# Kernel tuning notes

Measured on AMD Instinct MI355X. Metric: run time of the kernel, lower is better.

Reference implementation:

```python
import jax, jax.numpy as jnp
import numpy as np
from functools import partial

N_QUBITS = 4
N_LAYERS = 2
DIM = 2 ** N_QUBITS  # 16


def _conv(x, w, b):
    y = jax.lax.conv_general_dilated(
        x, w, window_strides=(1, 1), padding='SAME',
        dimension_numbers=('NCHW', 'OIHW', 'NCHW'))
    return y + b[None, :, None, None]


def _maxpool2(x):
    return jax.lax.reduce_window(
        x, -jnp.inf, jax.lax.max,
        window_dimensions=(1, 1, 2, 2), window_strides=(1, 1, 2, 2), padding='VALID')


def _rot_matrix(phi, theta, omega):
    # Rot = RZ(omega) @ RY(theta) @ RZ(phi)
    c = jnp.cos(theta / 2).astype(jnp.complex64)
    s = jnp.sin(theta / 2).astype(jnp.complex64)
    ep = jnp.exp(-0.5j * (phi + omega).astype(jnp.complex64))
    em = jnp.exp(0.5j * (phi - omega).astype(jnp.complex64))
    row0 = jnp.stack([ep * c, -em * s])
    row1 = jnp.stack([jnp.conj(em) * s, jnp.conj(ep) * c])
    return jnp.stack([row0, row1])  # [2,2]


def _quantum_circuit(feat16, q_weights):
    # feat16: [B,16] real; amplitude embedding with normalization
    B = feat16.shape[0]
    norm = jnp.linalg.norm(feat16, axis=1, keepdims=True)
    amps = feat16 / jnp.maximum(norm, 1e-12)
    state = amps.astype(jnp.complex64).reshape((B,) + (2,) * N_QUBITS)
    for layer in range(N_LAYERS):
        for q in range(N_QUBITS):
            U = _rot_matrix(q_weights[layer, q, 0], q_weights[layer, q, 1], q_weights[layer, q, 2])
            state = jnp.moveaxis(jnp.tensordot(U, state, axes=[[1], [q + 1]]), 0, q + 1)
        for q in range(N_QUBITS - 1):
            # CNOT control=q, target=q+1 (adjacent wires)
            s = state.reshape(B, 2 ** q, 2, 2, 2 ** (N_QUBITS - q - 2))
            s = s.at[:, :, 1].set(s[:, :, 1, ::-1])
            state = s.reshape((B,) + (2,) * N_QUBITS)
    probs = jnp.real(state * jnp.conj(state))  # [B,2,2,2,2]
    outs = []
    for q in range(N_QUBITS):
        axes = tuple(a for a in range(1, N_QUBITS + 1) if a != q + 1)
        p = probs.sum(axis=axes)  # [B,2]
        outs.append(p[:, 0] - p[:, 1])  # <Z_q>
    return jnp.stack(outs, axis=1)  # [B,4]


def _forward(x, conv1_w, conv1_b, conv2_w, conv2_b, fc1_w, fc1_b, fc2_w, fc2_b,
             fc3_w, fc3_b, q_weights, fc4_w, fc4_b):
    h = jax.nn.relu(_conv(x, conv1_w, conv1_b))
    h = _maxpool2(h)  # [B,32,14,14]
    h = jax.nn.relu(_conv(h, conv2_w, conv2_b))
    h = _maxpool2(h)  # [B,64,7,7]
    h = h.reshape(h.shape[0], 64 * 7 * 7)
    h = jax.nn.relu(h @ fc1_w.T + fc1_b)
    h = jax.nn.relu(h @ fc2_w.T + fc2_b)
    feat = jax.nn.relu(h @ fc3_w.T + fc3_b)  # [B,16]
    q_out = _quantum_circuit(feat, q_weights)  # [B,4]
    z = jnp.concatenate([feat, q_out], axis=1) @ fc4_w.T + fc4_b  # [B,10]
    return jax.nn.log_softmax(z, axis=1)


def setup_inputs() -> dict:
    key = jax.random.key(0)
    ks = jax.random.split(key, 16)
    B = 1024
    def g(k, shape, fan_in):
        return jax.random.normal(k, shape, dtype=jnp.float32) * (1.0 / np.sqrt(fan_in))
    return {
        'x': jax.random.normal(ks[0], (B, 1, 28, 28), dtype=jnp.float32),
        'conv1_w': g(ks[1], (32, 1, 3, 3), 9),
        'conv1_b': jnp.zeros((32,), jnp.float32),
        'conv2_w': g(ks[2], (64, 32, 3, 3), 32 * 9),
        'conv2_b': jnp.zeros((64,), jnp.float32),
        'fc1_w': g(ks[3], (128, 64 * 7 * 7), 64 * 7 * 7),
        'fc1_b': jnp.zeros((128,), jnp.float32),
        'fc2_w': g(ks[4], (64, 128), 128),
        'fc2_b': jnp.zeros((64,), jnp.float32),
        'fc3_w': g(ks[5], (16, 64), 64),
        'fc3_b': jnp.zeros((16,), jnp.float32),
        'q_weights': jax.random.normal(ks[6], (N_LAYERS, N_QUBITS, 3), dtype=jnp.float32),
        'fc4_w': g(ks[7], (10, 16 + N_QUBITS), 20),
        'fc4_b': jnp.zeros((10,), jnp.float32),
    }


def reference(x, conv1_w, conv1_b, conv2_w, conv2_b, fc1_w, fc1_b, fc2_w, fc2_b,
              fc3_w, fc3_b, q_weights, fc4_w, fc4_b):
    return _forward(x, conv1_w, conv1_b, conv2_w, conv2_b, fc1_w, fc1_b,
                    fc2_w, fc2_b, fc3_w, fc3_b, q_weights, fc4_w, fc4_b)
```

## Files before the change

kernel.cpp:

```cpp
#include <hip/hip_runtime.h>
#include <math.h>

typedef unsigned short ushort_t;
typedef unsigned int uint_t;
typedef __attribute__((ext_vector_type(8))) short short8v;
typedef __attribute__((ext_vector_type(4))) float float4v;
typedef __attribute__((ext_vector_type(4))) unsigned short ushort4v;

static __device__ __forceinline__ ushort_t f2bf(float f) {
    union { float f; uint_t u; } v; v.f = f;
    uint_t r = (v.u + 0x7FFFu + ((v.u >> 16) & 1u)) >> 16;
    return (ushort_t)r;
}
static __device__ __forceinline__ float bf2f(ushort_t u) {
    union { uint_t u; float f; } v; v.u = ((uint_t)u) << 16;
    return v.f;
}

__global__ __launch_bounds__(256) void k_conv(
    const float* __restrict__ x,
    const float* __restrict__ c1w, const float* __restrict__ c1b,
    const float* __restrict__ c2w, const float* __restrict__ c2b,
    const float* __restrict__ fc1w, ushort_t* __restrict__ wb,
    ushort_t* __restrict__ p2g)
{
    const int t = threadIdx.x;
    if (blockIdx.x >= 1024) {
        const int i = ((blockIdx.x - 1024)*256 + t) * 8;
        const float4 a = *(const float4*)(fc1w + i);
        const float4 b = *(const float4*)(fc1w + i + 4);
        short8v pk;
        pk[0]=(short)f2bf(a.x); pk[1]=(short)f2bf(a.y);
        pk[2]=(short)f2bf(a.z); pk[3]=(short)f2bf(a.w);
        pk[4]=(short)f2bf(b.x); pk[5]=(short)f2bf(b.y);
        pk[6]=(short)f2bf(b.z); pk[7]=(short)f2bf(b.w);
        *(short8v*)(wb + i) = pk;
        return;
    }

    __shared__ __align__(16) ushort_t p1cl[8192];
    __shared__ __align__(16) float img[900];

    const int b = blockIdx.x;
    const int lane = t & 63, wv = t >> 6;

    for (int i = t; i < 4096; i += 256) ((uint_t*)p1cl)[i] = 0u;
    for (int i = t; i < 900; i += 256) img[i] = 0.f;
    __syncthreads();
    const float* xi = x + (size_t)b * 784;
    for (int i = t; i < 784; i += 256)
        img[(i/28 + 1)*30 + (i%28 + 1)] = xi[i];
    __syncthreads();

    {
        const int ocb1 = wv*8;
        float wk[8][9], bv[8];
        #pragma unroll
        for (int o = 0; o < 8; ++o) {
            bv[o] = c1b[ocb1 + o];
            #pragma unroll
            for (int k = 0; k < 9; ++k) wk[o][k] = c1w[(ocb1 + o)*9 + k];
        }
        #pragma unroll
        for (int ch = 0; ch < 4; ++ch) {
            int pos = ch*64 + lane;
            const bool act = pos < 196;
            if (!act) pos = 195;
            const int qy = pos / 14, qx = pos % 14;
            const float* ib = img + (2*qy)*30 + 2*qx;
            float v[4][4];
            #pragma unroll
            for (int rr = 0; rr < 4; ++rr) {
                const float2 a = *(const float2*)(ib + rr*30);
                const float2 c = *(const float2*)(ib + rr*30 + 2);
                v[rr][0]=a.x; v[rr][1]=a.y; v[rr][2]=c.x; v[rr][3]=c.y;
            }
            short8v pk;
            #pragma unroll
            for (int o = 0; o < 8; ++o) {
                float m = 0.f;
                #pragma unroll
                for (int dy = 0; dy < 2; ++dy)
                #pragma unroll
                for (int dx = 0; dx < 2; ++dx) {
                    float acc = bv[o];
                    #pragma unroll
                    for (int ky = 0; ky < 3; ++ky)
                    #pragma unroll
                    for (int kx = 0; kx < 3; ++kx)
                        acc = fmaf(v[dy+ky][dx+kx], wk[o][ky*3+kx], acc);
                    m = fmaxf(m, acc);
                }
                pk[o] = (short)f2bf(m);
            }
            if (act) *(short8v*)&p1cl[wv*2048 + ((qy+1)*16 + (qx+1))*8] = pk;
        }
    }
    __syncthreads();

    {
        const int ocb = wv*16;
        const int col = lane & 15, g = lane >> 4;
        const int oc  = ocb + col;
        short8v bfr[9];
        #pragma unroll
        for (int j = 0; j < 8; ++j) {
            const float* wp = c2w + ((size_t)oc*32 + g*8 + j)*9;
            #pragma unroll
            for (int s = 0; s < 9; ++s) bfr[s][j] = (short)f2bf(wp[s]);
        }
        const float bv = c2b[oc];
        ushort_t* po = p2g + (size_t)b*3136;
        #pragma unroll 1
        for (int mt = 0; mt < 13; ++mt) {
            int row = mt*16 + col; if (row > 195) row = 195;
            const int q  = row >> 2;
            const int py = q / 7, px = q - py*7;
            const int y0 = 2*py + ((row>>1)&1), x0 = 2*px + (row&1);
            const ushort_t* ap = &p1cl[g*2048 + (y0*16 + x0)*8];
            float4v c0 = {bv, bv, bv, bv};
            float4v c1 = {0.f, 0.f, 0.f, 0.f};
            c0 = __builtin_amdgcn_mfma_f32_16x16x32_bf16(*(const short8v*)(ap +   0), bfr[0], c0, 0, 0, 0);
            c1 = __builtin_amdgcn_mfma_f32_16x16x32_bf16(*(const short8v*)(ap +   8), bfr[1], c1, 0, 0, 0);
            c0 = __builtin_amdgcn_mfma_f32_16x16x32_bf16(*(const short8v*)(ap +  16), bfr[2], c0, 0, 0, 0);
            c1 = __builtin_amdgcn_mfma_f32_16x16x32_bf16(*(const short8v*)(ap + 128), bfr[3], c1, 0, 0, 0);
            c0 = __builtin_amdgcn_mfma_f32_16x16x32_bf16(*(const short8v*)(ap + 136), bfr[4], c0, 0, 0, 0);
            c1 = __builtin_amdgcn_mfma_f32_16x16x32_bf16(*(const short8v*)(ap + 144), bfr[5], c1, 0, 0, 0);
            c0 = __builtin_amdgcn_mfma_f32_16x16x32_bf16(*(const short8v*)(ap + 256), bfr[6], c0, 0, 0, 0);
            c1 = __builtin_amdgcn_mfma_f32_16x16x32_bf16(*(const short8v*)(ap + 264), bfr[7], c1, 0, 0, 0);
            c0 = __builtin_amdgcn_mfma_f32_16x16x32_bf16(*(const short8v*)(ap + 272), bfr[8], c0, 0, 0, 0);
            const int quad = mt*4 + g;
            if (quad < 49) {
                const float m0 = fmaxf(fmaxf(c0[0]+c1[0], c0[1]+c1[1]),
                                       fmaxf(c0[2]+c1[2], c0[3]+c1[3]));
                po[oc*49 + quad] = f2bf(fmaxf(m0, 0.f));
            }
        }
    }
}

__global__ __launch_bounds__(256) void k_fc1(
    const ushort_t* __restrict__ p2g, const ushort_t* __restrict__ wb,
    const float* __restrict__ fc1b, float* __restrict__ h1g)
{
    __shared__ float cred[4][16][16];
    const int t = threadIdx.x, lane = t & 63, wv = t >> 6;
    const int imgT = blockIdx.x, ocT = blockIdx.y;
    const int sel = lane & 15, koff = (lane >> 4) * 8;
    const ushort_t* arow = p2g + (size_t)(imgT*16 + sel)*3136;
    const ushort_t* brow = wb  + (size_t)(ocT*16 + sel)*3136;
    const int n    = (wv < 2) ? 25 : 24;
    const int kbeg = wv*24 + (wv < 2 ? wv : 2);
    float4v c = {0.f, 0.f, 0.f, 0.f};
    int k0 = kbeg*32 + koff;
    short8v a0 = *(const short8v*)(arow + k0);
    short8v b0 = *(const short8v*)(brow + k0);
    for (int kk = 1; kk < n; ++kk) {
        const int k1 = (kbeg + kk)*32 + koff;
        const short8v a1 = *(const short8v*)(arow + k1);
        const short8v b1 = *(const short8v*)(brow + k1);
        c = __builtin_amdgcn_mfma_f32_16x16x32_bf16(a0, b0, c, 0, 0, 0);
        a0 = a1; b0 = b1;
    }
    c = __builtin_amdgcn_mfma_f32_16x16x32_bf16(a0, b0, c, 0, 0, 0);
    #pragma unroll
    for (int r = 0; r < 4; ++r) cred[wv][(lane>>4)*4 + r][sel] = c[r];
    __syncthreads();
    const int m = t >> 4, nn = t & 15;
    const float s = cred[0][m][nn] + cred[1][m][nn] + cred[2][m][nn] + cred[3][m][nn]
                  + fc1b[ocT*16 + nn];
    h1g[(size_t)(imgT*16 + m)*128 + ocT*16 + nn] = fmaxf(s, 0.f);
}

__global__ __launch_bounds__(64) void k_head(
    const float* __restrict__ h1,
    const float* __restrict__ fc2w, const float* __restrict__ fc2b,
    const float* __restrict__ fc3w, const float* __restrict__ fc3b,
    const float* __restrict__ qw,
    const float* __restrict__ fc4w, const float* __restrict__ fc4b,
    float* __restrict__ out)
{
    __shared__ float h1s[4][132];
    __shared__ float h2s[4][68];
    __shared__ float fs[4][16];
    __shared__ float zs[4][12];
    const int t = threadIdx.x;
    const int r = t >> 4, l = t & 15;
    const int b0 = blockIdx.x * 4;
    for (int i = t; i < 4*128; i += 64) h1s[i>>7][i&127] = h1[(size_t)b0*128 + i];
    __syncthreads();

    const int o0 = l*4;
    float a0 = fc2b[o0+0], a1 = fc2b[o0+1], a2 = fc2b[o0+2], a3 = fc2b[o0+3];
    #pragma unroll 4
    for (int k4 = 0; k4 < 32; ++k4) {
        const float4 h  = *(const float4*)&h1s[r][k4*4];
        const float4 w0 = *(const float4*)&fc2w[(o0+0)*128 + k4*4];
        const float4 w1 = *(const float4*)&fc2w[(o0+1)*128 + k4*4];
        const float4 w2 = *(const float4*)&fc2w[(o0+2)*128 + k4*4];
        const float4 w3 = *(const float4*)&fc2w[(o0+3)*128 + k4*4];
        a0 = fmaf(h.x,w0.x,fmaf(h.y,w0.y,fmaf(h.z,w0.z,fmaf(h.w,w0.w,a0))));
        a1 = fmaf(h.x,w1.x,fmaf(h.y,w1.y,fmaf(h.z,w1.z,fmaf(h.w,w1.w,a1))));
        a2 = fmaf(h.x,w2.x,fmaf(h.y,w2.y,fmaf(h.z,w2.z,fmaf(h.w,w2.w,a2))));
        a3 = fmaf(h.x,w3.x,fmaf(h.y,w3.y,fmaf(h.z,w3.z,fmaf(h.w,w3.w,a3))));
    }
    {
        float4 v = make_float4(fmaxf(a0,0.f), fmaxf(a1,0.f), fmaxf(a2,0.f), fmaxf(a3,0.f));
        *(float4*)&h2s[r][o0] = v;
    }
    __syncthreads();

    float facc = fc3b[l];
    #pragma unroll 4
    for (int k4 = 0; k4 < 16; ++k4) {
        const float4 h  = *(const float4*)&h2s[r][k4*4];
        const float4 wv = *(const float4*)&fc3w[l*64 + k4*4];
        facc = fmaf(h.x,wv.x,fmaf(h.y,wv.y,fmaf(h.z,wv.z,fmaf(h.w,wv.w,facc))));
    }
    const float feat = fmaxf(facc, 0.f);
    fs[r][l] = feat;

    float nrm2 = feat*feat;
    nrm2 += __shfl_xor(nrm2, 1);
    nrm2 += __shfl_xor(nrm2, 2);
    nrm2 += __shfl_xor(nrm2, 4);
    nrm2 += __shfl_xor(nrm2, 8);
    const float nrm = fmaxf(sqrtf(nrm2), 1e-12f);
    float re = feat / nrm, im = 0.f;
    #pragma unroll
    for (int layer = 0; layer < 2; ++layer) {
        #pragma unroll
        for (int q = 0; q < 4; ++q) {
            const float phi = qw[(layer*4 + q)*3 + 0];
            const float th  = qw[(layer*4 + q)*3 + 1];
            const float om  = qw[(layer*4 + q)*3 + 2];
            float st, ct; sincosf(0.5f*th, &st, &ct);
            float sa, ca; sincosf(0.5f*(phi + om), &sa, &ca);
            float sb, cb; sincosf(0.5f*(phi - om), &sb, &cb);
            const int pbit = 3 - q;
            const int bit  = (l >> pbit) & 1;
            const float pre = __shfl_xor(re, 1 << pbit);
            const float pim = __shfl_xor(im, 1 << pbit);
            const float sel = bit ? 1.f : -1.f;
            const float coR = ca*ct;
            const float coI = sel*sa*ct;
            const float cpR = sel*cb*st;
            const float cpI = -sb*st;
            const float nr = coR*re - coI*im + cpR*pre - cpI*pim;
            const float ni = coR*im + coI*re + cpR*pim + cpI*pre;
            re = nr; im = ni;
        }
        #pragma unroll
        for (int q = 0; q < 3; ++q) {
            const int cbit = 3 - q, tbit = 2 - q;
            const float sre = __shfl_xor(re, 1 << tbit);
            const float sim = __shfl_xor(im, 1 << tbit);
            if ((l >> cbit) & 1) { re = sre; im = sim; }
        }
    }
    const float pr = fmaf(re, re, im*im);
    float qo[4];
    #pragma unroll
    for (int q = 0; q < 4; ++q) {
        float v = ((l >> (3-q)) & 1) ? -pr : pr;
        v += __shfl_xor(v, 1);
        v += __shfl_xor(v, 2);
        v += __shfl_xor(v, 4);
        v += __shfl_xor(v, 8);
        qo[q] = v;
    }
    __syncthreads();

    if (l < 10) {
        float z = fc4b[l];
        #pragma unroll
        for (int j = 0; j < 16; ++j) z = fmaf(fs[r][j], fc4w[l*20 + j], z);
        #pragma unroll
        for (int j = 0; j < 4; ++j)  z = fmaf(qo[j], fc4w[l*20 + 16 + j], z);
        zs[r][l] = z;
        float mx = zs[r][0];
        #pragma unroll
        for (int j = 1; j < 10; ++j) mx = fmaxf(mx, zs[r][j]);
        float se = 0.f;
        #pragma unroll
        for (int j = 0; j < 10; ++j) se += expf(zs[r][j] - mx);
        out[(size_t)(b0 + r)*10 + l] = z - mx - logf(se);
    }
}

static __device__ __forceinline__ void circuit_head(
    const float* feat_in, const float* __restrict__ qw,
    const float* __restrict__ fc4w, const float* __restrict__ fc4b,
    float* __restrict__ outp)
{
    float feat[16];
    #pragma unroll
    for (int j = 0; j < 16; ++j) feat[j] = feat_in[j];
    float nrm2 = 0.f;
    #pragma unroll
    for (int j = 0; j < 16; ++j) nrm2 += feat[j]*feat[j];
    const float inv = 1.f / fmaxf(sqrtf(nrm2), 1e-12f);
    float ar[16], ai[16];
    #pragma unroll
    for (int j = 0; j < 16; ++j) { ar[j] = feat[j]*inv; ai[j] = 0.f; }
    #pragma unroll
    for (int layer = 0; layer < 2; ++layer) {
        #pragma unroll
        for (int q = 0; q < 4; ++q) {
            const float phi = qw[(layer*4 + q)*3 + 0];
            const float th  = qw[(layer*4 + q)*3 + 1];
            const float om  = qw[(layer*4 + q)*3 + 2];
            float st, ct; sincosf(0.5f*th, &st, &ct);
            float sa, ca; sincosf(0.5f*(phi + om), &sa, &ca);
            float sb, cb; sincosf(0.5f*(phi - om), &sb, &cb);
            const float U00r =  ca*ct, U00i = -sa*ct;
            const float U01r = -cb*st, U01i = -sb*st;
            const float U10r =  cb*st, U10i = -sb*st;
            const float U11r =  ca*ct, U11i =  sa*ct;
            const int stride = 1 << (3 - q);
            #pragma unroll
            for (int i0 = 0; i0 < 16; ++i0) {
                if (i0 & stride) continue;
                const int i1 = i0 | stride;
                const float r0 = ar[i0], m0 = ai[i0];
                const float r1 = ar[i1], m1 = ai[i1];
                ar[i0] = U00r*r0 - U00i*m0 + U01r*r1 - U01i*m1;
                ai[i0] = U00r*m0 + U00i*r0 + U01r*m1 + U01i*r1;
                ar[i1] = U10r*r0 - U10i*m0 + U11r*r1 - U11i*m1;
                ai[i1] = U10r*m0 + U10i*r0 + U11r*m1 + U11i*r1;
            }
        }
        #pragma unroll
        for (int q = 0; q < 3; ++q) {
            const int cbit = 1 << (3 - q), tbit = 1 << (2 - q);
            #pragma unroll
            for (int idx = 0; idx < 16; ++idx) {
                if ((idx & cbit) && !(idx & tbit)) {
                    const int j = idx | tbit;
                    float tr = ar[idx]; ar[idx] = ar[j]; ar[j] = tr;
                    float ti = ai[idx]; ai[idx] = ai[j]; ai[j] = ti;
                }
            }
        }
    }
    float qo[4];
    #pragma unroll
    for (int q = 0; q < 4; ++q) {
        const int pb = 1 << (3 - q);
        float s = 0.f;
        #pragma unroll
        for (int idx = 0; idx < 16; ++idx) {
            const float pv = ar[idx]*ar[idx] + ai[idx]*ai[idx];
            s += (idx & pb) ? -pv : pv;
        }
        qo[q] = s;
    }
    float z[10];
    float mx = -1e30f;
    #pragma unroll
    for (int o = 0; o < 10; ++o) {
        float a = fc4b[o];
        #pragma unroll
        for (int j = 0; j < 16; ++j) a = fmaf(feat[j], fc4w[o*20 + j], a);
        #pragma unroll
        for (int j = 0; j < 4;  ++j) a = fmaf(qo[j],  fc4w[o*20 + 16 + j], a);
        z[o] = a; mx = fmaxf(mx, a);
    }
    float se = 0.f;
    #pragma unroll
    for (int o = 0; o < 10; ++o) se += expf(z[o] - mx);
    const float lse = logf(se);
    #pragma unroll
    for (int o = 0; o < 10; ++o) outp[o] = z[o] - mx - lse;
}

__global__ __launch_bounds__(256) void k_fused_b(
    const float* __restrict__ x,
    const float* __restrict__ c1w, const float* __restrict__ c1b,
    const float* __restrict__ c2w, const float* __restrict__ c2b,
    const ushort_t* __restrict__ fc1wb, const float* __restrict__ fc1b,
    const float* __restrict__ fc2w, const float* __restrict__ fc2b,
    const float* __restrict__ fc3w, const float* __restrict__ fc3b,
    const float* __restrict__ qw,
    const float* __restrict__ fc4w, const float* __restrict__ fc4b,
    float* __restrict__ out)
{
    __shared__ __align__(16) ushort_t p1cl[8192];
    __shared__ __align__(16) float p2[3136];
    __shared__ float h1s[128];
    __shared__ float h2s[64];
    __shared__ float fts[16];

    const int b = blockIdx.x, t = threadIdx.x;
    const int lane = t & 63, wv = t >> 6;

    for (int i = t; i < 4096; i += 256) ((uint_t*)p1cl)[i] = 0u;
    float* img = p2;
    for (int i = t; i < 900; i += 256) img[i] = 0.f;
    __syncthreads();
    const float* xi = x + (size_t)b * 784;
    for (int i = t; i < 784; i += 256)
        img[(i/28 + 1)*30 + (i%28 + 1)] = xi[i];
    __syncthreads();

    {
        const int ocb1 = wv*8;
        float wk[8][9], bv[8];
        #pragma unroll
        for (int o = 0; o < 8; ++o) {
            bv[o] = c1b[ocb1 + o];
            #pragma unroll
            for (int k = 0; k < 9; ++k) wk[o][k] = c1w[(ocb1 + o)*9 + k];
        }
        #pragma unroll
        for (int ch = 0; ch < 4; ++ch) {
            int pos = ch*64 + lane;
            const bool act = pos < 196;
            if (!act) pos = 195;
            const int qy = pos / 14, qx = pos % 14;
            const float* ib = img + (2*qy)*30 + 2*qx;
            float v[4][4];
            #pragma unroll
            for (int rr = 0; rr < 4; ++rr) {
                const float2 a = *(const float2*)(ib + rr*30);
                const float2 c = *(const float2*)(ib + rr*30 + 2);
                v[rr][0]=a.x; v[rr][1]=a.y; v[rr][2]=c.x; v[rr][3]=c.y;
            }
            short8v pk;
            #pragma unroll
            for (int o = 0; o < 8; ++o) {
                float m = 0.f;
                #pragma unroll
                for (int dy = 0; dy < 2; ++dy)
                #pragma unroll
                for (int dx = 0; dx < 2; ++dx) {
                    float acc = bv[o];
                    #pragma unroll
                    for (int ky = 0; ky < 3; ++ky)
                    #pragma unroll
                    for (int kx = 0; kx < 3; ++kx)
                        acc = fmaf(v[dy+ky][dx+kx], wk[o][ky*3+kx], acc);
                    m = fmaxf(m, acc);
                }
                pk[o] = (short)f2bf(m);
            }
            if (act) *(short8v*)&p1cl[wv*2048 + ((qy+1)*16 + (qx+1))*8] = pk;
        }
    }
    __syncthreads();

    {
        const int ocb = wv*16;
        const int col = lane & 15, g = lane >> 4;
        const int oc  = ocb + col;
        short8v bfr[9];
        #pragma unroll
        for (int j = 0; j < 8; ++j) {
            const float* wp = c2w + ((size_t)oc*32 + g*8 + j)*9;
            #pragma unroll
            for (int s = 0; s < 9; ++s) bfr[s][j] = (short)f2bf(wp[s]);
        }
        const float bv = c2b[oc];
        #pragma unroll 1
        for (int mt = 0; mt < 13; ++mt) {
            int row = mt*16 + col; if (row > 195) row = 195;
            const int q  = row >> 2;
            const int py = q / 7, px = q - py*7;
            const int y0 = 2*py + ((row>>1)&1), x0 = 2*px + (row&1);
            const ushort_t* ap = &p1cl[g*2048 + (y0*16 + x0)*8];
            float4v c0 = {bv, bv, bv, bv};
            float4v c1 = {0.f, 0.f, 0.f, 0.f};
            c0 = __builtin_amdgcn_mfma_f32_16x16x32_bf16(*(const short8v*)(ap +   0), bfr[0], c0, 0, 0, 0);
            c1 = __builtin_amdgcn_mfma_f32_16x16x32_bf16(*(const short8v*)(ap +   8), bfr[1], c1, 0, 0, 0);
            c0 = __builtin_amdgcn_mfma_f32_16x16x32_bf16(*(const short8v*)(ap +  16), bfr[2], c0, 0, 0, 0);
            c1 = __builtin_amdgcn_mfma_f32_16x16x32_bf16(*(const short8v*)(ap + 128), bfr[3], c1, 0, 0, 0);
            c0 = __builtin_amdgcn_mfma_f32_16x16x32_bf16(*(const short8v*)(ap + 136), bfr[4], c0, 0, 0, 0);
            c1 = __builtin_amdgcn_mfma_f32_16x16x32_bf16(*(const short8v*)(ap + 144), bfr[5], c1, 0, 0, 0);
            c0 = __builtin_amdgcn_mfma_f32_16x16x32_bf16(*(const short8v*)(ap + 256), bfr[6], c0, 0, 0, 0);
            c1 = __builtin_amdgcn_mfma_f32_16x16x32_bf16(*(const short8v*)(ap + 264), bfr[7], c1, 0, 0, 0);
            c0 = __builtin_amdgcn_mfma_f32_16x16x32_bf16(*(const short8v*)(ap + 272), bfr[8], c0, 0, 0, 0);
            const int quad = mt*4 + g;
            if (quad < 49) {
                const float m0 = fmaxf(fmaxf(c0[0]+c1[0], c0[1]+c1[1]),
                                       fmaxf(c0[2]+c1[2], c0[3]+c1[3]));
                p2[oc*49 + quad] = fmaxf(m0, 0.f);
            }
        }
    }
    __syncthreads();

    for (int pass = 0; pass < 8; ++pass) {
        const int o = wv*32 + pass*4;
        const ushort_t* w0 = fc1wb + (size_t)o*3136;
        float a0=0.f, a1=0.f, a2=0.f, a3=0.f;
        #pragma unroll 2
        for (int kb = 0; kb < 3072; kb += 256) {
            const int k = kb + lane*4;
            const float4 pv = *(const float4*)&p2[k];
            const ushort4v u0 = *(const ushort4v*)(w0 + k);
            const ushort4v u1 = *(const ushort4v*)(w0 + 3136 + k);
            const ushort4v u2 = *(const ushort4v*)(w0 + 6272 + k);
            const ushort4v u3 = *(const ushort4v*)(w0 + 9408 + k);
            a0 = fmaf(pv.x,bf2f(u0[0]),fmaf(pv.y,bf2f(u0[1]),fmaf(pv.z,bf2f(u0[2]),fmaf(pv.w,bf2f(u0[3]),a0))));
            a1 = fmaf(pv.x,bf2f(u1[0]),fmaf(pv.y,bf2f(u1[1]),fmaf(pv.z,bf2f(u1[2]),fmaf(pv.w,bf2f(u1[3]),a1))));
            a2 = fmaf(pv.x,bf2f(u2[0]),fmaf(pv.y,bf2f(u2[1]),fmaf(pv.z,bf2f(u2[2]),fmaf(pv.w,bf2f(u2[3]),a2))));
            a3 = fmaf(pv.x,bf2f(u3[0]),fmaf(pv.y,bf2f(u3[1]),fmaf(pv.z,bf2f(u3[2]),fmaf(pv.w,bf2f(u3[3]),a3))));
        }
        if (lane < 16) {
            const int k = 3072 + lane*4;
            const float4 pv = *(const float4*)&p2[k];
            const ushort4v u0 = *(const ushort4v*)(w0 + k);
            const ushort4v u1 = *(const ushort4v*)(w0 + 3136 + k);
            const ushort4v u2 = *(const ushort4v*)(w0 + 6272 + k);
            const ushort4v u3 = *(const ushort4v*)(w0 + 9408 + k);
            a0 = fmaf(pv.x,bf2f(u0[0]),fmaf(pv.y,bf2f(u0[1]),fmaf(pv.z,bf2f(u0[2]),fmaf(pv.w,bf2f(u0[3]),a0))));
            a1 = fmaf(pv.x,bf2f(u1[0]),fmaf(pv.y,bf2f(u1[1]),fmaf(pv.z,bf2f(u1[2]),fmaf(pv.w,bf2f(u1[3]),a1))));
            a2 = fmaf(pv.x,bf2f(u2[0]),fmaf(pv.y,bf2f(u2[1]),fmaf(pv.z,bf2f(u2[2]),fmaf(pv.w,bf2f(u2[3]),a2))));
            a3 = fmaf(pv.x,bf2f(u3[0]),fmaf(pv.y,bf2f(u3[1]),fmaf(pv.z,bf2f(u3[2]),fmaf(pv.w,bf2f(u3[3]),a3))));
        }
        #pragma unroll
        for (int s = 1; s < 64; s <<= 1) {
            a0 += __shfl_xor(a0, s);
            a1 += __shfl_xor(a1, s);
            a2 += __shfl_xor(a2, s);
            a3 += __shfl_xor(a3, s);
        }
        if (lane == ((o+0)&63)) h1s[o+0] = fmaxf(a0 + fc1b[o+0], 0.f);
        if (lane == ((o+1)&63)) h1s[o+1] = fmaxf(a1 + fc1b[o+1], 0.f);
        if (lane == ((o+2)&63)) h1s[o+2] = fmaxf(a2 + fc1b[o+2], 0.f);
        if (lane == ((o+3)&63)) h1s[o+3] = fmaxf(a3 + fc1b[o+3], 0.f);
    }
    __syncthreads();

    if (t < 64) {
        float a = fc2b[t];
        const float* wr = fc2w + t * 128;
        for (int k = 0; k < 128; ++k) a = fmaf(h1s[k], wr[k], a);
        h2s[t] = fmaxf(a, 0.f);
    }
    __syncthreads();
    if (t < 16) {
        float a = fc3b[t];
        const float* wr = fc3w + t * 64;
        for (int k = 0; k < 64; ++k) a = fmaf(h2s[k], wr[k], a);
        fts[t] = fmaxf(a, 0.f);
    }
    __syncthreads();
    if (t == 0) circuit_head(fts, qw, fc4w, fc4b, out + (size_t)b*10);
}

__global__ __launch_bounds__(256) void k_cvtw_fb(
    const float* __restrict__ w, ushort_t* __restrict__ o)
{
    const int i = (blockIdx.x*256 + threadIdx.x) * 8;
    const float4 a = *(const float4*)(w + i);
    const float4 b = *(const float4*)(w + i + 4);
    short8v pk;
    pk[0]=(short)f2bf(a.x); pk[1]=(short)f2bf(a.y);
    pk[2]=(short)f2bf(a.z); pk[3]=(short)f2bf(a.w);
    pk[4]=(short)f2bf(b.x); pk[5]=(short)f2bf(b.y);
    pk[6]=(short)f2bf(b.z); pk[7]=(short)f2bf(b.w);
    *(short8v*)(o + i) = pk;
}

extern "C" void kernel_launch(void* const* d_in, const int* in_sizes, int n_in,
                              void* d_out, int out_size, void* d_ws, size_t ws_size,
                              hipStream_t stream) {
    const float* x     = (const float*)d_in[0];
    const float* c1w   = (const float*)d_in[1];
    const float* c1b   = (const float*)d_in[2];
    const float* c2w   = (const float*)d_in[3];
    const float* c2b   = (const float*)d_in[4];
    const float* fc1w  = (const float*)d_in[5];
    const float* fc1b  = (const float*)d_in[6];
    const float* fc2w  = (const float*)d_in[7];
    const float* fc2b  = (const float*)d_in[8];
    const float* fc3w  = (const float*)d_in[9];
    const float* fc3b  = (const float*)d_in[10];
    const float* qwp   = (const float*)d_in[11];
    const float* fc4w  = (const float*)d_in[12];
    const float* fc4b  = (const float*)d_in[13];
    float* outp = (float*)d_out;

    const size_t WB  = (size_t)128*3136*2;
    const size_t P2B = (size_t)1024*3136*2;
    const size_t H1B = (size_t)1024*128*4;

    if (ws_size >= WB + P2B + H1B) {
        ushort_t* wb  = (ushort_t*)d_ws;
        ushort_t* p2g = (ushort_t*)((char*)d_ws + WB);
        float*    h1g = (float*)((char*)d_ws + WB + P2B);
        k_conv<<<1220, 256, 0, stream>>>(x, c1w, c1b, c2w, c2b, fc1w, wb, p2g);
        k_fc1<<<dim3(64, 8), 256, 0, stream>>>(p2g, wb, fc1b, h1g);
        k_head<<<256, 64, 0, stream>>>(h1g, fc2w, fc2b, fc3w, fc3b, qwp,
                                       fc4w, fc4b, outp);
    } else if (ws_size >= WB) {
        ushort_t* wb = (ushort_t*)d_ws;
        k_cvtw_fb<<<196, 256, 0, stream>>>(fc1w, wb);
        k_fused_b<<<1024, 256, 0, stream>>>(x, c1w, c1b, c2w, c2b, wb, fc1b,
                                            fc2w, fc2b, fc3w, fc3b, qwp,
                                            fc4w, fc4b, outp);
    }
}
```

Baseline: 56.89 us.

## Fuse fc1 GEMM into head kernel, removing the h1 global round trip

Merges the fc1 MFMA GEMM and the fc2/fc3/quantum/fc4 head into one kernel with 64 blocks, each handling 16 images across all 128 fc1 outputs. The aim is to drop one kernel launch and the global write and read of the h1 activations. In exchange, the fc1 work runs on far fewer blocks. Each wave walks the full 98-step K loop with no K-split and no explicit prefetch, which lengthens the serial load-latency chain.

New measurement: 89.57 us. 57.4% more time.

```diff
diff --git a/kernel.cpp b/kernel.cpp
--- a/kernel.cpp
+++ b/kernel.cpp
@@ -139,56 +139,50 @@
     }
 }
 
-__global__ __launch_bounds__(256) void k_fc1(
+__global__ __launch_bounds__(256) void k_tail(
     const ushort_t* __restrict__ p2g, const ushort_t* __restrict__ wb,
-    const float* __restrict__ fc1b, float* __restrict__ h1g)
-{
-    __shared__ float cred[4][16][16];
-    const int t = threadIdx.x, lane = t & 63, wv = t >> 6;
-    const int imgT = blockIdx.x, ocT = blockIdx.y;
-    const int sel = lane & 15, koff = (lane >> 4) * 8;
-    const ushort_t* arow = p2g + (size_t)(imgT*16 + sel)*3136;
-    const ushort_t* brow = wb  + (size_t)(ocT*16 + sel)*3136;
-    const int n    = (wv < 2) ? 25 : 24;
-    const int kbeg = wv*24 + (wv < 2 ? wv : 2);
-    float4v c = {0.f, 0.f, 0.f, 0.f};
-    int k0 = kbeg*32 + koff;
-    short8v a0 = *(const short8v*)(arow + k0);
-    short8v b0 = *(const short8v*)(brow + k0);
-    for (int kk = 1; kk < n; ++kk) {
-        const int k1 = (kbeg + kk)*32 + koff;
-        const short8v a1 = *(const short8v*)(arow + k1);
-        const short8v b1 = *(const short8v*)(brow + k1);
-        c = __builtin_amdgcn_mfma_f32_16x16x32_bf16(a0, b0, c, 0, 0, 0);
-        a0 = a1; b0 = b1;
-    }
-    c = __builtin_amdgcn_mfma_f32_16x16x32_bf16(a0, b0, c, 0, 0, 0);
-    #pragma unroll
-    for (int r = 0; r < 4; ++r) cred[wv][(lane>>4)*4 + r][sel] = c[r];
-    __syncthreads();
-    const int m = t >> 4, nn = t & 15;
-    const float s = cred[0][m][nn] + cred[1][m][nn] + cred[2][m][nn] + cred[3][m][nn]
-                  + fc1b[ocT*16 + nn];
-    h1g[(size_t)(imgT*16 + m)*128 + ocT*16 + nn] = fmaxf(s, 0.f);
-}
-
-__global__ __launch_bounds__(64) void k_head(
-    const float* __restrict__ h1,
+    const float* __restrict__ fc1b,
     const float* __restrict__ fc2w, const float* __restrict__ fc2b,
     const float* __restrict__ fc3w, const float* __restrict__ fc3b,
     const float* __restrict__ qw,
     const float* __restrict__ fc4w, const float* __restrict__ fc4b,
     float* __restrict__ out)
 {
-    __shared__ float h1s[4][132];
-    __shared__ float h2s[4][68];
-    __shared__ float fs[4][16];
-    __shared__ float zs[4][12];
-    const int t = threadIdx.x;
+    __shared__ float h1s[16][132];
+    __shared__ float h2s[16][68];
+    __shared__ float fs[16][16];
+    __shared__ float zs[16][12];
+    const int t = threadIdx.x, lane = t & 63, wv = t >> 6;
+    const int imgT = blockIdx.x;
+    const int sel = lane & 15, koff = (lane >> 4) * 8;
+
+    {
+        const ushort_t* arow  = p2g + (size_t)(imgT*16 + sel)*3136;
+        const ushort_t* brow0 = wb  + (size_t)(wv*32      + sel)*3136;
+        const ushort_t* brow1 = wb  + (size_t)(wv*32 + 16 + sel)*3136;
+        float4v c0 = {0.f, 0.f, 0.f, 0.f};
+        float4v c1 = {0.f, 0.f, 0.f, 0.f};
+        for (int kk = 0; kk < 98; ++kk) {
+            const int k0 = kk*32 + koff;
+            const short8v a  = *(const short8v*)(arow  + k0);
+            const short8v b0 = *(const short8v*)(brow0 + k0);
+            const short8v b1 = *(const short8v*)(brow1 + k0);
+            c0 = __builtin_amdgcn_mfma_f32_16x16x32_bf16(a, b0, c0, 0, 0, 0);
+            c1 = __builtin_amdgcn_mfma_f32_16x16x32_bf16(a, b1, c1, 0, 0, 0);
+        }
+        const float bv0 = fc1b[wv*32 + sel];
+        const float bv1 = fc1b[wv*32 + 16 + sel];
+        #pragma unroll
+        for (int r = 0; r < 4; ++r) {
+            const int im = (lane>>4)*4 + r;
+            h1s[im][wv*32 + sel]      = fmaxf(c0[r] + bv0, 0.f);
+            h1s[im][wv*32 + 16 + sel] = fmaxf(c1[r] + bv1, 0.f);
+        }
+    }
+    __syncthreads();
+
     const int r = t >> 4, l = t & 15;
-    const int b0 = blockIdx.x * 4;
-    for (int i = t; i < 4*128; i += 64) h1s[i>>7][i&127] = h1[(size_t)b0*128 + i];
-    __syncthreads();
+    const int b0 = imgT * 16;
 
     const int o0 = l*4;
     float a0 = fc2b[o0+0], a1 = fc2b[o0+1], a2 = fc2b[o0+2], a3 = fc2b[o0+3];
@@ -214,8 +208,8 @@
     #pragma unroll 4
     for (int k4 = 0; k4 < 16; ++k4) {
         const float4 h  = *(const float4*)&h2s[r][k4*4];
-        const float4 wv = *(const float4*)&fc3w[l*64 + k4*4];
-        facc = fmaf(h.x,wv.x,fmaf(h.y,wv.y,fmaf(h.z,wv.z,fmaf(h.w,wv.w,facc))));
+        const float4 wv4 = *(const float4*)&fc3w[l*64 + k4*4];
+        facc = fmaf(h.x,wv4.x,fmaf(h.y,wv4.y,fmaf(h.z,wv4.z,fmaf(h.w,wv4.w,facc))));
     }
     const float feat = fmaxf(facc, 0.f);
     fs[r][l] = feat;
@@ -241,10 +235,10 @@
             const int bit  = (l >> pbit) & 1;
             const float pre = __shfl_xor(re, 1 << pbit);
             const float pim = __shfl_xor(im, 1 << pbit);
-            const float sel = bit ? 1.f : -1.f;
+            const float selv = bit ? 1.f : -1.f;
             const float coR = ca*ct;
-            const float coI = sel*sa*ct;
-            const float cpR = sel*cb*st;
+            const float coI = selv*sa*ct;
+            const float cpR = selv*cb*st;
             const float cpI = -sb*st;
             const float nr = coR*re - coI*im + cpR*pre - cpI*pim;
             const float ni = coR*im + coI*re + cpR*pim + cpI*pre;
@@ -584,16 +578,13 @@
 
     const size_t WB  = (size_t)128*3136*2;
     const size_t P2B = (size_t)1024*3136*2;
-    const size_t H1B = (size_t)1024*128*4;
-
-    if (ws_size >= WB + P2B + H1B) {
+
+    if (ws_size >= WB + P2B) {
         ushort_t* wb  = (ushort_t*)d_ws;
         ushort_t* p2g = (ushort_t*)((char*)d_ws + WB);
-        float*    h1g = (float*)((char*)d_ws + WB + P2B);
         k_conv<<<1220, 256, 0, stream>>>(x, c1w, c1b, c2w, c2b, fc1w, wb, p2g);
-        k_fc1<<<dim3(64, 8), 256, 0, stream>>>(p2g, wb, fc1b, h1g);
-        k_head<<<256, 64, 0, stream>>>(h1g, fc2w, fc2b, fc3w, fc3b, qwp,
-                                       fc4w, fc4b, outp);
+        k_tail<<<64, 256, 0, stream>>>(p2g, wb, fc1b, fc2w, fc2b, fc3w, fc3b,
+                                       qwp, fc4w, fc4b, outp);
     } else if (ws_size >= WB) {
         ushort_t* wb = (ushort_t*)d_ws;
         k_cvtw_fb<<<196, 256, 0, stream>>>(fc1w, wb);
```
